# Performance work log

Hardware: AMD Instinct MI355X
Metric: run time of the kernel (lower is better)

The kernel has to match this reference:

```python
import jax, jax.numpy as jnp
import numpy as np

B, T, F = 4096, 72, 9
H = 64            # GRU units per direction
DENSE = 128
P = 24            # predict_window


def _gru_scan(xp, h0, U, br, act):
    """xp: (T,B,3H) precomputed input projections; Keras reset_after=True GRU."""
    def step(h, x_t):
        rec = h @ U + br                      # (B,3H)
        xz, xr, xh = jnp.split(x_t, 3, axis=-1)
        rz, rr, rh = jnp.split(rec, 3, axis=-1)
        z = jax.nn.sigmoid(xz + rz)
        r = jax.nn.sigmoid(xr + rr)
        hh = act(xh + r * rh)
        h_new = z * h + (1.0 - z) * hh
        return h_new, h_new
    hT, hs = jax.lax.scan(step, h0, xp)
    return hT, hs


def _bigru(x, h0f, h0b, Wf, Uf, bif, brf, Wb, Ub, bib, brb, act, return_sequences):
    xt = jnp.swapaxes(x, 0, 1)                # (T,B,F)
    xpf = xt @ Wf + bif                       # (T,B,3H)
    xpb = xt[::-1] @ Wb + bib                 # reversed time for backward dir
    hTf, hsf = _gru_scan(xpf, h0f, Uf, brf, act)
    hTb, hsb = _gru_scan(xpb, h0b, Ub, brb, act)
    if return_sequences:
        out = jnp.concatenate([hsf, hsb[::-1]], axis=-1)   # (T,B,2H)
        return jnp.swapaxes(out, 0, 1)                      # (B,T,2H)
    return jnp.concatenate([hTf, hTb], axis=-1)             # (B,2H)


def _glorot(key, shape):
    fan_in, fan_out = shape[0], shape[-1]
    lim = np.sqrt(6.0 / (fan_in + fan_out))
    return jax.random.uniform(key, shape, jnp.float32, -lim, lim)


def setup_inputs() -> dict:
    key = jax.random.key(0)
    ks = jax.random.split(key, 16)
    d = {
        "x": jax.random.normal(ks[0], (B, T, F), jnp.float32),
        "h0_fwd": jnp.zeros((B, H), jnp.float32),
        "h0_bwd": jnp.zeros((B, H), jnp.float32),
        # d1 (input F=9), forward & backward directions
        "d1f_W": _glorot(ks[1], (F, 3 * H)), "d1f_U": _glorot(ks[2], (H, 3 * H)),
        "d1f_bi": jnp.zeros((3 * H,), jnp.float32), "d1f_br": jnp.zeros((3 * H,), jnp.float32),
        "d1b_W": _glorot(ks[3], (F, 3 * H)), "d1b_U": _glorot(ks[4], (H, 3 * H)),
        "d1b_bi": jnp.zeros((3 * H,), jnp.float32), "d1b_br": jnp.zeros((3 * H,), jnp.float32),
        # d2 (input 2H=128)
        "d2f_W": _glorot(ks[5], (2 * H, 3 * H)), "d2f_U": _glorot(ks[6], (H, 3 * H)),
        "d2f_bi": jnp.zeros((3 * H,), jnp.float32), "d2f_br": jnp.zeros((3 * H,), jnp.float32),
        "d2b_W": _glorot(ks[7], (2 * H, 3 * H)), "d2b_U": _glorot(ks[8], (H, 3 * H)),
        "d2b_bi": jnp.zeros((3 * H,), jnp.float32), "d2b_br": jnp.zeros((3 * H,), jnp.float32),
        # dense heads
        "dense_W": _glorot(ks[9], (2 * H, DENSE)), "dense_b": jnp.zeros((DENSE,), jnp.float32),
        "out_W": _glorot(ks[10], (DENSE, P)), "out_b": jnp.zeros((P,), jnp.float32),
    }
    return d


def reference(x, h0_fwd, h0_bwd,
              d1f_W, d1f_U, d1f_bi, d1f_br, d1b_W, d1b_U, d1b_bi, d1b_br,
              d2f_W, d2f_U, d2f_bi, d2f_br, d2b_W, d2b_U, d2b_bi, d2b_br,
              dense_W, dense_b, out_W, out_b):
    # d1: Bidirectional GRU(64, activation=relu), return_sequences=True, initial_state=hidden
    seq = _bigru(x, h0_fwd, h0_bwd,
                 d1f_W, d1f_U, d1f_bi, d1f_br,
                 d1b_W, d1b_U, d1b_bi, d1b_br,
                 jax.nn.relu, True)                         # (B,T,128)
    # d2: Bidirectional GRU(64, activation=tanh), zero initial state, last-state output
    z0 = jnp.zeros((x.shape[0], H), seq.dtype)
    feat = _bigru(seq, z0, z0,
                  d2f_W, d2f_U, d2f_bi, d2f_br,
                  d2b_W, d2b_U, d2b_bi, d2b_br,
                  jnp.tanh, False)                          # (B,128)
    h = jax.nn.relu(feat @ dense_W + dense_b)               # (B,128)
    out = jax.nn.softmax(h @ out_W + out_b, axis=-1)        # (B,P)
    return out
```

## Files before the change

kernel.cpp:

```cpp
#include <hip/hip_runtime.h>
#include <hip/hip_bf16.h>

typedef __attribute__((ext_vector_type(8))) short short8;
typedef __attribute__((ext_vector_type(4))) float f32x4;
typedef unsigned short ush;

#define MFMA_B16(a, b, c) __builtin_amdgcn_mfma_f32_16x16x32_bf16((a), (b), (c), 0, 0, 0)

__device__ __forceinline__ float bf2f(ush u) {
    union { unsigned int i; float f; } v; v.i = ((unsigned int)u) << 16; return v.f;
}
__device__ __forceinline__ ush f2bf(float f) {
    union { float f; unsigned int i; } v; v.f = f;
    unsigned int r = v.i + 0x7fffu + ((v.i >> 16) & 1u);
    return (ush)(r >> 16);
}
__device__ __forceinline__ float rcp_f(float x) { return __builtin_amdgcn_rcpf(x); }
__device__ __forceinline__ float sigm_pre(float x) {
    return rcp_f(1.0f + __builtin_amdgcn_exp2f(x));
}
__device__ __forceinline__ float tanh_pre(float x) {
    return 1.0f - 2.0f * rcp_f(__builtin_amdgcn_exp2f(x) + 1.0f);
}

__device__ __forceinline__ void lds_barrier() {
    asm volatile("s_waitcnt lgkmcnt(0)" ::: "memory");
    __builtin_amdgcn_s_barrier();
    asm volatile("" ::: "memory");
}

__device__ __forceinline__ bool probe_bf16(const ush* p, int tid, int* s_cnt) {
    if (tid == 0) *s_cnt = 0;
    __syncthreads();
    ush s = p[tid & 255];
    int e = (s >> 7) & 0xFF;
    if (tid < 256 && e >= 117 && e <= 137) atomicAdd(s_cnt, 1);
    __syncthreads();
    return *s_cnt >= 200;
}

struct WArgs {
    const void* src[20];
    int off[21];
};

__global__ __launch_bounds__(256)
void convert_w(WArgs a, ush* __restrict__ arena, const ush* __restrict__ probe)
{
    __shared__ int cnt;
    const bool bf = probe_bf16(probe, threadIdx.x, &cnt);
    const int total = a.off[20];
    for (int i = blockIdx.x * 256 + threadIdx.x; i < total; i += gridDim.x * 256) {
        int t = 0;
        while (t < 19 && i >= a.off[t + 1]) ++t;
        const int local = i - a.off[t];
        float v = bf ? bf2f(((const ush*)a.src[t])[local])
                     : ((const float*)a.src[t])[local];
        if (t < 16) {
            const int col = local % 192;
            if (col < 128) v *= -1.4426950408889634f;
            else if (t >= 8) v *= 2.885390081777927f;
        }
        arena[i] = f2bf(v);
    }
}

__global__ __launch_bounds__(256, 1)
void gru1_kernel(const void* __restrict__ X, const void* __restrict__ h0f,
                 const void* __restrict__ h0b, int cb, int bchunk,
                 const ush* __restrict__ Wf, const ush* __restrict__ Uf,
                 const ush* __restrict__ bif, const ush* __restrict__ brf,
                 const ush* __restrict__ Wb, const ush* __restrict__ Ub,
                 const ush* __restrict__ bib, const ush* __restrict__ brb,
                 ush* __restrict__ seq)
{
    const int tid  = threadIdx.x;
    const int lane = tid & 63;
    const int wv   = tid >> 6;
    const int q    = lane >> 4;
    const int ln   = lane & 15;
    const int dir  = blockIdx.y;
    const int lb0  = blockIdx.x * 16;
    const int gb0  = cb + lb0;
    const int u    = wv * 16 + ln;

    const ush* W  = dir ? Wb  : Wf;
    const ush* U  = dir ? Ub  : Uf;
    const ush* bi = dir ? bib : bif;
    const ush* br = dir ? brb : brf;
    const void* h0 = dir ? h0b : h0f;

    __shared__ __align__(16) ush Ah[2][16][72];
    __shared__ __align__(16) ush Ax[2][16][40];
    __shared__ int s_cnt;

    const bool xbf = probe_bf16((const ush*)X, tid, &s_cnt);

    {
        ush* p = &Ax[0][0][0];
        for (int i = tid; i < 2 * 16 * 40; i += 256) p[i] = 0;
    }
    __syncthreads();

    {
        const int tx0 = dir ? 71 : 0;
        if (tid < 144) {
            int r = tid / 9, k = tid - 9 * r;
            size_t idx = ((size_t)(gb0 + r) * 72 + tx0) * 9 + k;
            ush hv, lv;
            if (xbf) { hv = ((const ush*)X)[idx]; lv = 0; }
            else { float v = ((const float*)X)[idx]; hv = f2bf(v); lv = f2bf(v - bf2f(hv)); }
            Ax[0][r][2 * k]     = hv;
            Ax[0][r][2 * k + 1] = lv;
        }
    }

    short8 bU[3][2];
    short8 bW[3];
#pragma unroll
    for (int g = 0; g < 3; ++g) {
        const int col = g * 64 + u;
#pragma unroll
        for (int ks = 0; ks < 2; ++ks) {
            short8 f;
#pragma unroll
            for (int j = 0; j < 8; ++j) {
                int kp = ks * 32 + q * 8 + j;
                f[j] = (short)U[(size_t)kp * 192 + col];
            }
            bU[g][ks] = f;
        }
        short8 fw;
#pragma unroll
        for (int j = 0; j < 8; ++j) {
            int kp = q * 8 + j;
            fw[j] = (kp < 18) ? (short)W[(size_t)(kp >> 1) * 192 + col] : (short)0;
        }
        bW[g] = fw;
    }

    const float bz  = bf2f(bi[u])       + bf2f(br[u]);
    const float brg = bf2f(bi[64 + u])  + bf2f(br[64 + u]);
    const float bih = bf2f(bi[128 + u]);
    const float brh = bf2f(br[128 + u]);
    const f32x4 Cz  = {bz,  bz,  bz,  bz};
    const f32x4 Cr  = {brg, brg, brg, brg};
    const f32x4 Chx = {bih, bih, bih, bih};
    const f32x4 Chr = {brh, brh, brh, brh};

    float hreg[4];
#pragma unroll
    for (int i = 0; i < 4; ++i) {
        int m = q * 4 + i;
        size_t idx = (size_t)(gb0 + m) * 64 + u;
        float hv = xbf ? bf2f(((const ush*)h0)[idx])
                       : ((const float*)h0)[idx];
        hreg[i] = hv;
        Ah[0][m][u] = f2bf(hv);
    }

    const int r2 = tid >> 3, c2 = tid & 7;
    const int r0x = tid / 9, k0x = tid - 9 * r0x;

    unsigned int craw = 0;
    if (tid < 144) {
        const int tx = dir ? 70 : 1;
        size_t idx = ((size_t)(gb0 + r0x) * 72 + tx) * 9 + k0x;
        craw = xbf ? (unsigned int)((const ush*)X)[idx]
                   : ((const unsigned int*)X)[idx];
    }
    __syncthreads();

#pragma unroll 2
    for (int t = 0; t < 72; ++t) {
        const int cur = t & 1, nb = cur ^ 1;

        unsigned int fraw = 0;
        if (t < 70 && tid < 144) {
            const int tx = dir ? (69 - t) : (t + 2);
            size_t idx = ((size_t)(gb0 + r0x) * 72 + tx) * 9 + k0x;
            fraw = xbf ? (unsigned int)((const ush*)X)[idx]
                       : ((const unsigned int*)X)[idx];
        }

        if (t > 0 && tid < 128) {
            const int tw = dir ? (71 - (t - 1)) : (t - 1);
            int4 v = *(const int4*)&Ah[cur][r2][c2 * 8];
            *(int4*)(seq + ((size_t)tw * bchunk + lb0 + r2) * 128 + dir * 64 + c2 * 8) = v;
        }

        const ush* ap = &Ah[cur][ln][0];
        short8 a0 = *(const short8*)(ap + q * 8);
        short8 a1 = *(const short8*)(ap + 32 + q * 8);
        short8 ax = *(const short8*)(&Ax[cur][ln][q * 8]);
        f32x4 az  = MFMA_B16(ax, bW[0], Cz);
        az        = MFMA_B16(a0, bU[0][0], az);
        az        = MFMA_B16(a1, bU[0][1], az);
        f32x4 ar  = MFMA_B16(ax, bW[1], Cr);
        ar        = MFMA_B16(a0, bU[1][0], ar);
        ar        = MFMA_B16(a1, bU[1][1], ar);
        f32x4 ahx = MFMA_B16(ax, bW[2], Chx);
        f32x4 ahr = MFMA_B16(a0, bU[2][0], Chr);
        ahr       = MFMA_B16(a1, bU[2][1], ahr);

#pragma unroll
        for (int i = 0; i < 4; ++i) {
            const int m = q * 4 + i;
            float z = sigm_pre(az[i]);
            float r = sigm_pre(ar[i]);
            float pre = ahx[i] + r * ahr[i];
            float hh = fmaxf(pre, 0.0f);
            float hn = hh + z * (hreg[i] - hh);
            hreg[i] = hn;
            Ah[nb][m][u] = f2bf(hn);
        }

        if (t < 71 && tid < 144) {
            ush hv, lv;
            if (xbf) { hv = (ush)craw; lv = 0; }
            else {
                float v = __uint_as_float(craw);
                hv = f2bf(v); lv = f2bf(v - bf2f(hv));
            }
            Ax[nb][r0x][2 * k0x]     = hv;
            Ax[nb][r0x][2 * k0x + 1] = lv;
        }
        craw = fraw;
        lds_barrier();
    }

    if (tid < 128) {
        const int tw = dir ? 0 : 71;
        int4 v = *(const int4*)&Ah[0][r2][c2 * 8];
        *(int4*)(seq + ((size_t)tw * bchunk + lb0 + r2) * 128 + dir * 64 + c2 * 8) = v;
    }
}

#define PCOMPUTE(E, BUFI)                                                      \
    do {                                                                       \
        f32x4 p0 = MFMA_B16(E##0, bV[0][0], Cg0);                              \
        p0 = MFMA_B16(E##1, bV[0][1], p0);                                     \
        p0 = MFMA_B16(E##2, bV[0][2], p0);                                     \
        p0 = MFMA_B16(E##3, bV[0][3], p0);                                     \
        *(f32x4*)&Pbuf[BUFI][0][pn][poff] = p0;                                \
        f32x4 p1 = MFMA_B16(E##0, bV[1][0], Cg1);                              \
        p1 = MFMA_B16(E##1, bV[1][1], p1);                                     \
        p1 = MFMA_B16(E##2, bV[1][2], p1);                                     \
        p1 = MFMA_B16(E##3, bV[1][3], p1);                                     \
        *(f32x4*)&Pbuf[BUFI][1][pn][poff] = p1;                                \
        f32x4 p2 = MFMA_B16(E##0, bV[2][0], Cg2);                              \
        p2 = MFMA_B16(E##1, bV[2][1], p2);                                     \
        p2 = MFMA_B16(E##2, bV[2][2], p2);                                     \
        p2 = MFMA_B16(E##3, bV[2][3], p2);                                     \
        *(f32x4*)&Pbuf[BUFI][2][pn][poff] = p2;                                \
    } while (0)

#define ELOAD(E, T)                                                            \
    do {                                                                       \
        const ush* sp_ = sptr0 + (long long)(T) * tstride;                     \
        E##0 = *(const short8*)(sp_);                                          \
        E##1 = *(const short8*)(sp_ + 32);                                     \
        E##2 = *(const short8*)(sp_ + 64);                                     \
        E##3 = *(const short8*)(sp_ + 96);                                     \
    } while (0)

__global__ __launch_bounds__(512, 1)
void gru2_kernel(const ush* __restrict__ seq, int cb, int bchunk,
                 const ush* __restrict__ W2f, const ush* __restrict__ U2f,
                 const ush* __restrict__ bi2f, const ush* __restrict__ br2f,
                 const ush* __restrict__ W2b, const ush* __restrict__ U2b,
                 const ush* __restrict__ bi2b, const ush* __restrict__ br2b,
                 float* __restrict__ feat)
{
    const int tid  = threadIdx.x;
    const int wv   = tid >> 6;
    const int lane = tid & 63;
    const int q    = lane >> 4;
    const int ln   = lane & 15;
    const int dir  = blockIdx.y;
    const int lb0  = blockIdx.x * 16;
    const int gb0  = cb + lb0;

    const ush* W  = dir ? W2b  : W2f;
    const ush* U  = dir ? U2b  : U2f;
    const ush* bi = dir ? bi2b : bi2f;
    const ush* br = dir ? br2b : br2f;

    __shared__ __align__(16) float Pbuf[2][3][4][288];
    __shared__ __align__(16) ush Ah[2][16][72];

    const int poff = (lane >> 3) * 36 + (lane & 7) * 4;

    if (wv < 4) {
        const int pn = wv;
        const int u2 = pn * 16 + ln;

        short8 bV[3][4];
#pragma unroll
        for (int g = 0; g < 3; ++g) {
            const int col = g * 64 + u2;
#pragma unroll
            for (int ks = 0; ks < 4; ++ks) {
                short8 f;
#pragma unroll
                for (int j = 0; j < 8; ++j) {
                    int kp = ks * 32 + q * 8 + j;
                    f[j] = (short)W[(size_t)kp * 192 + col];
                }
                bV[g][ks] = f;
            }
        }
        const float bz  = bf2f(bi[u2]) + bf2f(br[u2]);
        const float brg = bf2f(bi[64 + u2]) + bf2f(br[64 + u2]);
        const float bih = bf2f(bi[128 + u2]);
        const f32x4 Cg0 = {bz, bz, bz, bz};
        const f32x4 Cg1 = {brg, brg, brg, brg};
        const f32x4 Cg2 = {bih, bih, bih, bih};

        const long long tstride = (long long)bchunk * 128 * (dir ? -1 : 1);
        const ush* sptr0 = seq + (size_t)(lb0 + ln) * 128 + q * 8
                         + (dir ? 71ll * bchunk * 128 : 0);

        short8 EA0, EA1, EA2, EA3, EB0, EB1, EB2, EB3;
        ELOAD(EA, 0);
        PCOMPUTE(EA, 0);
        ELOAD(EA, 1);
        ELOAD(EB, 2);
        lds_barrier();

        for (int t = 0; t < 72; t += 2) {
            PCOMPUTE(EA, 1);
            if (t <= 68) ELOAD(EA, t + 3);
            lds_barrier();
            if (t + 1 < 71) PCOMPUTE(EB, 0);
            if (t + 1 <= 68) ELOAD(EB, t + 4);
            lds_barrier();
        }
    } else {
        const int cn = wv - 4;
        const int u2 = cn * 16 + ln;

        short8 bU[3][2];
#pragma unroll
        for (int g = 0; g < 3; ++g) {
            const int col = g * 64 + u2;
#pragma unroll
            for (int ks = 0; ks < 2; ++ks) {
                short8 f;
#pragma unroll
                for (int j = 0; j < 8; ++j) {
                    int kp = ks * 32 + q * 8 + j;
                    f[j] = (short)U[(size_t)kp * 192 + col];
                }
                bU[g][ks] = f;
            }
        }
        const float brh = bf2f(br[128 + u2]);
        const f32x4 Chr = {brh, brh, brh, brh};

        for (int i = tid - 256; i < 16 * 72; i += 256) (&Ah[0][0][0])[i] = 0;
        float hreg[4];
#pragma unroll
        for (int i = 0; i < 4; ++i) hreg[i] = 0.0f;
        lds_barrier();

        for (int t = 0; t < 72; ++t) {
            const int cur = t & 1, nb = cur ^ 1;

            f32x4 Pz = *(const f32x4*)&Pbuf[cur][0][cn][poff];
            f32x4 Pr = *(const f32x4*)&Pbuf[cur][1][cn][poff];
            f32x4 Pc = *(const f32x4*)&Pbuf[cur][2][cn][poff];

            const ush* ap = &Ah[cur][ln][0];
            short8 a0 = *(const short8*)(ap + q * 8);
            short8 a1 = *(const short8*)(ap + 32 + q * 8);

            f32x4 az  = MFMA_B16(a0, bU[0][0], Pz);
            az        = MFMA_B16(a1, bU[0][1], az);
            f32x4 ar  = MFMA_B16(a0, bU[1][0], Pr);
            ar        = MFMA_B16(a1, bU[1][1], ar);
            f32x4 ahr = MFMA_B16(a0, bU[2][0], Chr);
            ahr       = MFMA_B16(a1, bU[2][1], ahr);

#pragma unroll
            for (int i = 0; i < 4; ++i) {
                const int m = q * 4 + i;
                float z = sigm_pre(az[i]);
                float r = sigm_pre(ar[i]);
                float pre = Pc[i] + r * ahr[i];
                float hh = tanh_pre(pre);
                float hn = hh + z * (hreg[i] - hh);
                hreg[i] = hn;
                Ah[nb][m][u2] = f2bf(hn);
            }
            lds_barrier();
        }

#pragma unroll
        for (int i = 0; i < 4; ++i) {
            const int m = q * 4 + i;
            feat[(size_t)(gb0 + m) * 128 + dir * 64 + u2] = hreg[i];
        }
    }
}

__global__ __launch_bounds__(256, 1)
void head_kernel(const float* __restrict__ feat,
                 const ush* __restrict__ dW, const ush* __restrict__ db,
                 const ush* __restrict__ oW, const ush* __restrict__ ob,
                 float* __restrict__ out)
{
    const int tid = threadIdx.x;
    const int b0  = blockIdx.x * 16;

    __shared__ __align__(16) ush Wl[128][136];
    __shared__ __align__(16) float fs[16][128];
    __shared__ __align__(16) float hs[16][136];
    __shared__ __align__(16) float ls[16][32];

    for (int i = tid; i < 2048; i += 256) {
        const int k = i >> 4;
        const int c = (i & 15) * 8;
        *(int4*)&Wl[k][c] = *(const int4*)(dW + (size_t)k * 128 + c);
    }
    {
        const float4* src = (const float4*)(feat + (size_t)b0 * 128);
        float4* dst = (float4*)&fs[0][0];
        for (int i = tid; i < 512; i += 256) dst[i] = src[i];
    }
    __syncthreads();

    {
        const int row = tid >> 4;
        const int j0  = (tid & 15) * 8;
        float acc[8];
#pragma unroll
        for (int jj = 0; jj < 8; ++jj) acc[jj] = bf2f(db[j0 + jj]);
        for (int k = 0; k < 128; ++k) {
            float f = fs[row][k];
            short8 w = *(const short8*)&Wl[k][j0];
#pragma unroll
            for (int jj = 0; jj < 8; ++jj)
                acc[jj] += f * bf2f((ush)w[jj]);
        }
#pragma unroll
        for (int jj = 0; jj < 8; ++jj) hs[row][j0 + jj] = fmaxf(acc[jj], 0.0f);
    }
    __syncthreads();

    for (int e = tid; e < 16 * 24; e += 256) {
        const int row = e / 24, l = e - 24 * row;
        float acc = bf2f(ob[l]);
        for (int k = 0; k < 128; ++k)
            acc += hs[row][k] * bf2f(oW[(size_t)k * 24 + l]);
        ls[row][l] = acc;
    }
    __syncthreads();

    for (int e = tid; e < 16 * 24; e += 256) {
        const int row = e / 24, l = e - 24 * row;
        float mx = ls[row][0];
#pragma unroll
        for (int k = 1; k < 24; ++k) mx = fmaxf(mx, ls[row][k]);
        float s = 0.0f;
#pragma unroll
        for (int k = 0; k < 24; ++k) s += __expf(ls[row][k] - mx);
        float v = __expf(ls[row][l] - mx) * rcp_f(s);
        out[(size_t)(b0 + row) * 24 + l] = v;
    }
}

extern "C" void kernel_launch(void* const* d_in, const int* in_sizes, int n_in,
                              void* d_out, int out_size, void* d_ws, size_t ws_size,
                              hipStream_t stream) {
    (void)in_sizes; (void)n_in; (void)out_size;

    static const int wc[20] = {
        1728, 12288, 192, 192,
        1728, 12288, 192, 192,
        24576, 12288, 192, 192,
        24576, 12288, 192, 192,
        16384, 128,
        3072, 24
    };

    WArgs a;
    int off = 0;
    for (int t = 0; t < 20; ++t) {
        a.src[t] = d_in[t + 3];
        a.off[t] = off;
        off += wc[t];
    }
    a.off[20] = off;

    const unsigned long long arena_bytes = 245952ull;
    const unsigned long long feat_bytes  = 4096ull * 128ull * 4ull;
    const unsigned long long seq_full    = 72ull * 4096ull * 128ull * 2ull;
    const unsigned long long fixed       = arena_bytes + feat_bytes;

    int nc = 32;
    for (int c = 1; c <= 32; c *= 2) {
        if (fixed + seq_full / (unsigned long long)c <= (unsigned long long)ws_size) { nc = c; break; }
    }
    const int bchunk = 4096 / nc;

    ush* arena  = (ush*)d_ws;
    float* feat = (float*)((char*)d_ws + arena_bytes);
    ush* seq    = (ush*)((char*)d_ws + fixed);

    convert_w<<<128, 256, 0, stream>>>(a, arena, (const ush*)d_in[0]);

    const ush* d1fW = arena + a.off[0];
    const ush* d1fU = arena + a.off[1];
    const ush* d1fbi= arena + a.off[2];
    const ush* d1fbr= arena + a.off[3];
    const ush* d1bW = arena + a.off[4];
    const ush* d1bU = arena + a.off[5];
    const ush* d1bbi= arena + a.off[6];
    const ush* d1bbr= arena + a.off[7];
    const ush* d2fW = arena + a.off[8];
    const ush* d2fU = arena + a.off[9];
    const ush* d2fbi= arena + a.off[10];
    const ush* d2fbr= arena + a.off[11];
    const ush* d2bW = arena + a.off[12];
    const ush* d2bU = arena + a.off[13];
    const ush* d2bbi= arena + a.off[14];
    const ush* d2bbr= arena + a.off[15];
    const ush* dW   = arena + a.off[16];
    const ush* db   = arena + a.off[17];
    const ush* oW   = arena + a.off[18];
    const ush* ob   = arena + a.off[19];

    for (int c = 0; c < nc; ++c) {
        const int cb = c * bchunk;
        gru1_kernel<<<dim3(bchunk / 16, 2), 256, 0, stream>>>(
            d_in[0], d_in[1], d_in[2], cb, bchunk,
            d1fW, d1fU, d1fbi, d1fbr, d1bW, d1bU, d1bbi, d1bbr, seq);
        gru2_kernel<<<dim3(bchunk / 16, 2), 512, 0, stream>>>(
            seq, cb, bchunk,
            d2fW, d2fU, d2fbi, d2fbr, d2bW, d2bU, d2bbi, d2bbr, feat);
    }
    head_kernel<<<256, 256, 0, stream>>>(
        feat, dW, db, oW, ob, (float*)d_out);
}
```

Measured before the change: 242.6 us.

## Merge gru2 producer/consumer warps into single 256-thread recurrent loop

After: 245.6 us. About the same (+1.3%).

```diff
diff --git a/kernel.cpp b/kernel.cpp
--- a/kernel.cpp
+++ b/kernel.cpp
@@ -90,15 +90,15 @@
     const ush* br = dir ? brb : brf;
     const void* h0 = dir ? h0b : h0f;
 
-    __shared__ __align__(16) ush Ah[2][16][72];
-    __shared__ __align__(16) ush Ax[2][16][40];
+    __shared__ __align__(16) ush Ah[2][16][76];
+    __shared__ __align__(16) ush Ax[2][16][44];
     __shared__ int s_cnt;
 
     const bool xbf = probe_bf16((const ush*)X, tid, &s_cnt);
 
     {
         ush* p = &Ax[0][0][0];
-        for (int i = tid; i < 2 * 16 * 40; i += 256) p[i] = 0;
+        for (int i = tid; i < 2 * 16 * 44; i += 256) p[i] = 0;
     }
     __syncthreads();
 
@@ -236,35 +236,54 @@
     }
 }
 
-#define PCOMPUTE(E, BUFI)                                                      \
+#define G2STEP(T, S0, S1, S2, S3)                                              \
     do {                                                                       \
-        f32x4 p0 = MFMA_B16(E##0, bV[0][0], Cg0);                              \
-        p0 = MFMA_B16(E##1, bV[0][1], p0);                                     \
-        p0 = MFMA_B16(E##2, bV[0][2], p0);                                     \
-        p0 = MFMA_B16(E##3, bV[0][3], p0);                                     \
-        *(f32x4*)&Pbuf[BUFI][0][pn][poff] = p0;                                \
-        f32x4 p1 = MFMA_B16(E##0, bV[1][0], Cg1);                              \
-        p1 = MFMA_B16(E##1, bV[1][1], p1);                                     \
-        p1 = MFMA_B16(E##2, bV[1][2], p1);                                     \
-        p1 = MFMA_B16(E##3, bV[1][3], p1);                                     \
-        *(f32x4*)&Pbuf[BUFI][1][pn][poff] = p1;                                \
-        f32x4 p2 = MFMA_B16(E##0, bV[2][0], Cg2);                              \
-        p2 = MFMA_B16(E##1, bV[2][1], p2);                                     \
-        p2 = MFMA_B16(E##2, bV[2][2], p2);                                     \
-        p2 = MFMA_B16(E##3, bV[2][3], p2);                                     \
-        *(f32x4*)&Pbuf[BUFI][2][pn][poff] = p2;                                \
+        const int cur_ = (T) & 1, nb_ = cur_ ^ 1;                              \
+        const ush* ap_ = &Ah[cur_][ln][0];                                     \
+        short8 a0 = *(const short8*)(ap_ + q * 8);                             \
+        short8 a1 = *(const short8*)(ap_ + 32 + q * 8);                        \
+        f32x4 az  = MFMA_B16(a0, bU[0][0], P0);                                \
+        az        = MFMA_B16(a1, bU[0][1], az);                                \
+        f32x4 ar  = MFMA_B16(a0, bU[1][0], P1);                                \
+        ar        = MFMA_B16(a1, bU[1][1], ar);                                \
+        f32x4 ahr = MFMA_B16(a0, bU[2][0], Chr);                               \
+        ahr       = MFMA_B16(a1, bU[2][1], ahr);                               \
+        f32x4 ahx = P2;                                                        \
+        _Pragma("unroll") for (int i = 0; i < 4; ++i) {                        \
+            const int m = q * 4 + i;                                           \
+            float z = sigm_pre(az[i]);                                         \
+            float r = sigm_pre(ar[i]);                                         \
+            float pre = ahx[i] + r * ahr[i];                                   \
+            float hh = tanh_pre(pre);                                          \
+            float hn = hh + z * (hreg[i] - hh);                                \
+            hreg[i] = hn;                                                      \
+            Ah[nb_][m][u] = f2bf(hn);                                          \
+        }                                                                      \
+        if ((T) < 71) {               \
+            P0 = MFMA_B16(S0, bV[0][0], Cz);                                   \
+            P0 = MFMA_B16(S1, bV[0][1], P0);                                   \
+            P0 = MFMA_B16(S2, bV[0][2], P0);                                   \
+            P0 = MFMA_B16(S3, bV[0][3], P0);                                   \
+            P1 = MFMA_B16(S0, bV[1][0], Cr);                                   \
+            P1 = MFMA_B16(S1, bV[1][1], P1);                                   \
+            P1 = MFMA_B16(S2, bV[1][2], P1);                                   \
+            P1 = MFMA_B16(S3, bV[1][3], P1);                                   \
+            P2 = MFMA_B16(S0, bV[2][0], Chx);                                  \
+            P2 = MFMA_B16(S1, bV[2][1], P2);                                   \
+            P2 = MFMA_B16(S2, bV[2][2], P2);                                   \
+            P2 = MFMA_B16(S3, bV[2][3], P2);                                   \
+        }                                                                      \
+        if ((T) <= 67) {                       \
+            const ush* sp_ = sptr0 + (long long)((T) + 4) * tstride;           \
+            S0 = *(const short8*)(sp_);                                        \
+            S1 = *(const short8*)(sp_ + 32);                                   \
+            S2 = *(const short8*)(sp_ + 64);                                   \
+            S3 = *(const short8*)(sp_ + 96);                                   \
+        }                                                                      \
+        lds_barrier();                                                         \
     } while (0)
 
-#define ELOAD(E, T)                                                            \
-    do {                                                                       \
-        const ush* sp_ = sptr0 + (long long)(T) * tstride;                     \
-        E##0 = *(const short8*)(sp_);                                          \
-        E##1 = *(const short8*)(sp_ + 32);                                     \
-        E##2 = *(const short8*)(sp_ + 64);                                     \
-        E##3 = *(const short8*)(sp_ + 96);                                     \
-    } while (0)
-
-__global__ __launch_bounds__(512, 1)
+__global__ __launch_bounds__(256, 1)
 void gru2_kernel(const ush* __restrict__ seq, int cb, int bchunk,
                  const ush* __restrict__ W2f, const ush* __restrict__ U2f,
                  const ush* __restrict__ bi2f, const ush* __restrict__ br2f,
@@ -273,134 +292,119 @@
                  float* __restrict__ feat)
 {
     const int tid  = threadIdx.x;
+    const int lane = tid & 63;
     const int wv   = tid >> 6;
-    const int lane = tid & 63;
     const int q    = lane >> 4;
     const int ln   = lane & 15;
     const int dir  = blockIdx.y;
     const int lb0  = blockIdx.x * 16;
     const int gb0  = cb + lb0;
+    const int u    = wv * 16 + ln;
 
     const ush* W  = dir ? W2b  : W2f;
     const ush* U  = dir ? U2b  : U2f;
     const ush* bi = dir ? bi2b : bi2f;
     const ush* br = dir ? br2b : br2f;
 
-    __shared__ __align__(16) float Pbuf[2][3][4][288];
-    __shared__ __align__(16) ush Ah[2][16][72];
-
-    const int poff = (lane >> 3) * 36 + (lane & 7) * 4;
-
-    if (wv < 4) {
-        const int pn = wv;
-        const int u2 = pn * 16 + ln;
-
-        short8 bV[3][4];
-#pragma unroll
-        for (int g = 0; g < 3; ++g) {
-            const int col = g * 64 + u2;
-#pragma unroll
-            for (int ks = 0; ks < 4; ++ks) {
-                short8 f;
-#pragma unroll
-                for (int j = 0; j < 8; ++j) {
-                    int kp = ks * 32 + q * 8 + j;
-                    f[j] = (short)W[(size_t)kp * 192 + col];
-                }
-                bV[g][ks] = f;
+    __shared__ __align__(16) ush Ah[2][16][76];
+
+    {
+        ush* p = &Ah[0][0][0];
+        for (int i = tid; i < 16 * 76; i += 256) p[i] = 0;
+    }
+
+    const long long tstride = (long long)bchunk * 128 * (dir ? -1 : 1);
+    const ush* sptr0 = seq + ((size_t)(lb0 + ln)) * 128 + q * 8
+                     + (dir ? 71ll * bchunk * 128 : 0);
+
+    short8 bU[3][2];
+    short8 bV[3][4];
+#pragma unroll
+    for (int g = 0; g < 3; ++g) {
+        const int col = g * 64 + u;
+#pragma unroll
+        for (int ks = 0; ks < 2; ++ks) {
+            short8 f;
+#pragma unroll
+            for (int j = 0; j < 8; ++j) {
+                int kp = ks * 32 + q * 8 + j;
+                f[j] = (short)U[(size_t)kp * 192 + col];
             }
-        }
-        const float bz  = bf2f(bi[u2]) + bf2f(br[u2]);
-        const float brg = bf2f(bi[64 + u2]) + bf2f(br[64 + u2]);
-        const float bih = bf2f(bi[128 + u2]);
-        const f32x4 Cg0 = {bz, bz, bz, bz};
-        const f32x4 Cg1 = {brg, brg, brg, brg};
-        const f32x4 Cg2 = {bih, bih, bih, bih};
-
-        const long long tstride = (long long)bchunk * 128 * (dir ? -1 : 1);
-        const ush* sptr0 = seq + (size_t)(lb0 + ln) * 128 + q * 8
-                         + (dir ? 71ll * bchunk * 128 : 0);
-
-        short8 EA0, EA1, EA2, EA3, EB0, EB1, EB2, EB3;
-        ELOAD(EA, 0);
-        PCOMPUTE(EA, 0);
-        ELOAD(EA, 1);
-        ELOAD(EB, 2);
-        lds_barrier();
-
-        for (int t = 0; t < 72; t += 2) {
-            PCOMPUTE(EA, 1);
-            if (t <= 68) ELOAD(EA, t + 3);
-            lds_barrier();
-            if (t + 1 < 71) PCOMPUTE(EB, 0);
-            if (t + 1 <= 68) ELOAD(EB, t + 4);
-            lds_barrier();
-        }
-    } else {
-        const int cn = wv - 4;
-        const int u2 = cn * 16 + ln;
-
-        short8 bU[3][2];
-#pragma unroll
-        for (int g = 0; g < 3; ++g) {
-            const int col = g * 64 + u2;
-#pragma unroll
-            for (int ks = 0; ks < 2; ++ks) {
-                short8 f;
-#pragma unroll
-                for (int j = 0; j < 8; ++j) {
-                    int kp = ks * 32 + q * 8 + j;
-                    f[j] = (short)U[(size_t)kp * 192 + col];
-                }
-                bU[g][ks] = f;
+            bU[g][ks] = f;
+        }
+#pragma unroll
+        for (int ks = 0; ks < 4; ++ks) {
+            short8 fv;
+#pragma unroll
+            for (int j = 0; j < 8; ++j) {
+                int kp = ks * 32 + q * 8 + j;
+                fv[j] = (short)W[(size_t)kp * 192 + col];
             }
-        }
-        const float brh = bf2f(br[128 + u2]);
-        const f32x4 Chr = {brh, brh, brh, brh};
-
-        for (int i = tid - 256; i < 16 * 72; i += 256) (&Ah[0][0][0])[i] = 0;
-        float hreg[4];
-#pragma unroll
-        for (int i = 0; i < 4; ++i) hreg[i] = 0.0f;
-        lds_barrier();
-
-        for (int t = 0; t < 72; ++t) {
-            const int cur = t & 1, nb = cur ^ 1;
-
-            f32x4 Pz = *(const f32x4*)&Pbuf[cur][0][cn][poff];
-            f32x4 Pr = *(const f32x4*)&Pbuf[cur][1][cn][poff];
-            f32x4 Pc = *(const f32x4*)&Pbuf[cur][2][cn][poff];
-
-            const ush* ap = &Ah[cur][ln][0];
-            short8 a0 = *(const short8*)(ap + q * 8);
-            short8 a1 = *(const short8*)(ap + 32 + q * 8);
-
-            f32x4 az  = MFMA_B16(a0, bU[0][0], Pz);
-            az        = MFMA_B16(a1, bU[0][1], az);
-            f32x4 ar  = MFMA_B16(a0, bU[1][0], Pr);
-            ar        = MFMA_B16(a1, bU[1][1], ar);
-            f32x4 ahr = MFMA_B16(a0, bU[2][0], Chr);
-            ahr       = MFMA_B16(a1, bU[2][1], ahr);
-
-#pragma unroll
-            for (int i = 0; i < 4; ++i) {
-                const int m = q * 4 + i;
-                float z = sigm_pre(az[i]);
-                float r = sigm_pre(ar[i]);
-                float pre = Pc[i] + r * ahr[i];
-                float hh = tanh_pre(pre);
-                float hn = hh + z * (hreg[i] - hh);
-                hreg[i] = hn;
-                Ah[nb][m][u2] = f2bf(hn);
-            }
-            lds_barrier();
-        }
-
-#pragma unroll
-        for (int i = 0; i < 4; ++i) {
-            const int m = q * 4 + i;
-            feat[(size_t)(gb0 + m) * 128 + dir * 64 + u2] = hreg[i];
-        }
+            bV[g][ks] = fv;
+        }
+    }
+
+    const float bz  = bf2f(bi[u])       + bf2f(br[u]);
+    const float brg = bf2f(bi[64 + u])  + bf2f(br[64 + u]);
+    const float bih = bf2f(bi[128 + u]);
+    const float brh = bf2f(br[128 + u]);
+    const f32x4 Cz  = {bz,  bz,  bz,  bz};
+    const f32x4 Cr  = {brg, brg, brg, brg};
+    const f32x4 Chx = {bih, bih, bih, bih};
+    const f32x4 Chr = {brh, brh, brh, brh};
+
+    float hreg[4];
+#pragma unroll
+    for (int i = 0; i < 4; ++i) hreg[i] = 0.0f;
+
+    f32x4 P0, P1, P2;
+    {
+        const ush* sp = sptr0;
+        short8 s0 = *(const short8*)(sp);
+        short8 s1 = *(const short8*)(sp + 32);
+        short8 s2 = *(const short8*)(sp + 64);
+        short8 s3 = *(const short8*)(sp + 96);
+        P0 = MFMA_B16(s0, bV[0][0], Cz);
+        P0 = MFMA_B16(s1, bV[0][1], P0);
+        P0 = MFMA_B16(s2, bV[0][2], P0);
+        P0 = MFMA_B16(s3, bV[0][3], P0);
+        P1 = MFMA_B16(s0, bV[1][0], Cr);
+        P1 = MFMA_B16(s1, bV[1][1], P1);
+        P1 = MFMA_B16(s2, bV[1][2], P1);
+        P1 = MFMA_B16(s3, bV[1][3], P1);
+        P2 = MFMA_B16(s0, bV[2][0], Chx);
+        P2 = MFMA_B16(s1, bV[2][1], P2);
+        P2 = MFMA_B16(s2, bV[2][2], P2);
+        P2 = MFMA_B16(s3, bV[2][3], P2);
+    }
+    short8 A0, A1, A2, A3, B0, B1, B2, B3, D0, D1, D2, D3;
+    {
+        const ush* sp = sptr0 + tstride;
+        A0 = *(const short8*)(sp);        A1 = *(const short8*)(sp + 32);
+        A2 = *(const short8*)(sp + 64);   A3 = *(const short8*)(sp + 96);
+    }
+    {
+        const ush* sp = sptr0 + 2 * tstride;
+        B0 = *(const short8*)(sp);        B1 = *(const short8*)(sp + 32);
+        B2 = *(const short8*)(sp + 64);   B3 = *(const short8*)(sp + 96);
+    }
+    {
+        const ush* sp = sptr0 + 3 * tstride;
+        D0 = *(const short8*)(sp);        D1 = *(const short8*)(sp + 32);
+        D2 = *(const short8*)(sp + 64);   D3 = *(const short8*)(sp + 96);
+    }
+    __syncthreads();
+
+    for (int t = 0; t < 72; t += 3) {
+        G2STEP(t,     A0, A1, A2, A3);
+        G2STEP(t + 1, B0, B1, B2, B3);
+        G2STEP(t + 2, D0, D1, D2, D3);
+    }
+
+#pragma unroll
+    for (int i = 0; i < 4; ++i) {
+        const int m = q * 4 + i;
+        feat[(size_t)(gb0 + m) * 128 + dir * 64 + u] = hreg[i];
     }
 }
 
@@ -536,7 +540,7 @@
         gru1_kernel<<<dim3(bchunk / 16, 2), 256, 0, stream>>>(
             d_in[0], d_in[1], d_in[2], cb, bchunk,
             d1fW, d1fU, d1fbi, d1fbr, d1bW, d1bU, d1bbi, d1bbr, seq);
-        gru2_kernel<<<dim3(bchunk / 16, 2), 512, 0, stream>>>(
+        gru2_kernel<<<dim3(bchunk / 16, 2), 256, 0, stream>>>(
             seq, cb, bchunk,
             d2fW, d2fU, d2fbi, d2fbr, d2bW, d2bU, d2bbi, d2bbr, feat);
     }
```

## Shrink GRU2 blocks to one producer and one consumer wave

Applied to the files above, without the earlier changes.

New measurement: 251.4 us. +3.6%, slower.

```diff
diff --git a/kernel.cpp b/kernel.cpp
--- a/kernel.cpp
+++ b/kernel.cpp
@@ -18,9 +18,6 @@
 __device__ __forceinline__ float rcp_f(float x) { return __builtin_amdgcn_rcpf(x); }
 __device__ __forceinline__ float sigm_pre(float x) {
     return rcp_f(1.0f + __builtin_amdgcn_exp2f(x));
-}
-__device__ __forceinline__ float tanh_pre(float x) {
-    return 1.0f - 2.0f * rcp_f(__builtin_amdgcn_exp2f(x) + 1.0f);
 }
 
 __device__ __forceinline__ void lds_barrier() {
@@ -90,15 +87,15 @@
     const ush* br = dir ? brb : brf;
     const void* h0 = dir ? h0b : h0f;
 
-    __shared__ __align__(16) ush Ah[2][16][72];
-    __shared__ __align__(16) ush Ax[2][16][40];
+    __shared__ __align__(16) ush Ah[2][16][76];
+    __shared__ __align__(16) ush Ax[2][16][44];
     __shared__ int s_cnt;
 
     const bool xbf = probe_bf16((const ush*)X, tid, &s_cnt);
 
     {
         ush* p = &Ax[0][0][0];
-        for (int i = tid; i < 2 * 16 * 40; i += 256) p[i] = 0;
+        for (int i = tid; i < 2 * 16 * 44; i += 256) p[i] = 0;
     }
     __syncthreads();
 
@@ -236,35 +233,61 @@
     }
 }
 
-#define PCOMPUTE(E, BUFI)                                                      \
+#define PROD_STEP(FA, BUFI, T)                                                 \
     do {                                                                       \
-        f32x4 p0 = MFMA_B16(E##0, bV[0][0], Cg0);                              \
-        p0 = MFMA_B16(E##1, bV[0][1], p0);                                     \
-        p0 = MFMA_B16(E##2, bV[0][2], p0);                                     \
-        p0 = MFMA_B16(E##3, bV[0][3], p0);                                     \
-        *(f32x4*)&Pbuf[BUFI][0][pn][poff] = p0;                                \
-        f32x4 p1 = MFMA_B16(E##0, bV[1][0], Cg1);                              \
-        p1 = MFMA_B16(E##1, bV[1][1], p1);                                     \
-        p1 = MFMA_B16(E##2, bV[1][2], p1);                                     \
-        p1 = MFMA_B16(E##3, bV[1][3], p1);                                     \
-        *(f32x4*)&Pbuf[BUFI][1][pn][poff] = p1;                                \
-        f32x4 p2 = MFMA_B16(E##0, bV[2][0], Cg2);                              \
-        p2 = MFMA_B16(E##1, bV[2][1], p2);                                     \
-        p2 = MFMA_B16(E##2, bV[2][2], p2);                                     \
-        p2 = MFMA_B16(E##3, bV[2][3], p2);                                     \
-        *(f32x4*)&Pbuf[BUFI][2][pn][poff] = p2;                                \
+        if ((T) < 71) {                                                        \
+            _Pragma("unroll") for (int g = 0; g < 3; ++g) {                    \
+                _Pragma("unroll") for (int n = 0; n < 4; ++n) {                \
+                    f32x4 acc = MFMA_B16(FA[0], bV[g][0][n], Cg[g][n]);        \
+                    acc = MFMA_B16(FA[1], bV[g][1][n], acc);                   \
+                    acc = MFMA_B16(FA[2], bV[g][2][n], acc);                   \
+                    acc = MFMA_B16(FA[3], bV[g][3][n], acc);                   \
+                    *(f32x4*)&Pbuf[BUFI][g][n][poff] = acc;                    \
+                }                                                              \
+            }                                                                  \
+        }                                                                      \
+        if ((T) < 69) {                                                        \
+            const ush* sp = sptr0 + (long long)((T) + 3) * tstride;            \
+            FA[0] = *(const short8*)sp;                                        \
+            FA[1] = *(const short8*)(sp + 32);                                 \
+            FA[2] = *(const short8*)(sp + 64);                                 \
+            FA[3] = *(const short8*)(sp + 96);                                 \
+        }                                                                      \
     } while (0)
 
-#define ELOAD(E, T)                                                            \
+#define CONS_STEP(BUFI, T)                                                     \
     do {                                                                       \
-        const ush* sp_ = sptr0 + (long long)(T) * tstride;                     \
-        E##0 = *(const short8*)(sp_);                                          \
-        E##1 = *(const short8*)(sp_ + 32);                                     \
-        E##2 = *(const short8*)(sp_ + 64);                                     \
-        E##3 = *(const short8*)(sp_ + 96);                                     \
+        f32x4 Pz[4], Pr[4], Pc[4];                                             \
+        _Pragma("unroll") for (int n = 0; n < 4; ++n) {                        \
+            Pz[n] = *(const f32x4*)&Pbuf[BUFI][0][n][poff];                    \
+            Pr[n] = *(const f32x4*)&Pbuf[BUFI][1][n][poff];                    \
+            Pc[n] = *(const f32x4*)&Pbuf[BUFI][2][n][poff];                    \
+        }                                                                      \
+        short8 a0 = *(const short8*)&Ah[ln][q * 8];                            \
+        short8 a1 = *(const short8*)&Ah[ln][32 + q * 8];                       \
+        f32x4 az[4], ar[4], ahr[4];                                            \
+        _Pragma("unroll") for (int n = 0; n < 4; ++n) {                        \
+            az[n]  = MFMA_B16(a0, bU[0][0][n], Pz[n]);                         \
+            az[n]  = MFMA_B16(a1, bU[0][1][n], az[n]);                         \
+            ar[n]  = MFMA_B16(a0, bU[1][0][n], Pr[n]);                         \
+            ar[n]  = MFMA_B16(a1, bU[1][1][n], ar[n]);                         \
+            ahr[n] = MFMA_B16(a0, bU[2][0][n], Chr[n]);                        \
+            ahr[n] = MFMA_B16(a1, bU[2][1][n], ahr[n]);                        \
+        }                                                                      \
+        _Pragma("unroll") for (int n = 0; n < 4; ++n)                          \
+            _Pragma("unroll") for (int i = 0; i < 4; ++i) {                    \
+                float z = sigm_pre(az[n][i]);                                  \
+                float r = sigm_pre(ar[n][i]);                                  \
+                float pre = Pc[n][i] + r * ahr[n][i];                          \
+                float e = __builtin_amdgcn_exp2f(pre);         \
+                float hh = 1.0f - 2.0f * rcp_f(e + 1.0f);                      \
+                float hn = hh + z * (hreg[n][i] - hh);                         \
+                hreg[n][i] = hn;                                               \
+                Ah[q * 4 + i][n * 16 + ln] = f2bf(hn);                         \
+            }                                                                  \
     } while (0)
 
-__global__ __launch_bounds__(512, 1)
+__global__ __launch_bounds__(128, 1)
 void gru2_kernel(const ush* __restrict__ seq, int cb, int bchunk,
                  const ush* __restrict__ W2f, const ush* __restrict__ U2f,
                  const ush* __restrict__ bi2f, const ush* __restrict__ br2f,
@@ -272,14 +295,9 @@
                  const ush* __restrict__ bi2b, const ush* __restrict__ br2b,
                  float* __restrict__ feat)
 {
-    const int tid  = threadIdx.x;
-    const int wv   = tid >> 6;
-    const int lane = tid & 63;
-    const int q    = lane >> 4;
-    const int ln   = lane & 15;
-    const int dir  = blockIdx.y;
-    const int lb0  = blockIdx.x * 16;
-    const int gb0  = cb + lb0;
+    const int tid = threadIdx.x;
+    const int wv = tid >> 6, lane = tid & 63, q = lane >> 4, ln = lane & 15;
+    const int dir = blockIdx.y, lb0 = blockIdx.x * 16, gb0 = cb + lb0;
 
     const ush* W  = dir ? W2b  : W2f;
     const ush* U  = dir ? U2b  : U2f;
@@ -287,120 +305,125 @@
     const ush* br = dir ? br2b : br2f;
 
     __shared__ __align__(16) float Pbuf[2][3][4][288];
-    __shared__ __align__(16) ush Ah[2][16][72];
+    __shared__ __align__(16) ush Ah[16][72];
 
     const int poff = (lane >> 3) * 36 + (lane & 7) * 4;
 
-    if (wv < 4) {
-        const int pn = wv;
-        const int u2 = pn * 16 + ln;
-
-        short8 bV[3][4];
-#pragma unroll
-        for (int g = 0; g < 3; ++g) {
-            const int col = g * 64 + u2;
-#pragma unroll
-            for (int ks = 0; ks < 4; ++ks) {
-                short8 f;
-#pragma unroll
-                for (int j = 0; j < 8; ++j) {
-                    int kp = ks * 32 + q * 8 + j;
-                    f[j] = (short)W[(size_t)kp * 192 + col];
+    if (wv == 0) {
+        short8 bV[3][4][4];
+#pragma unroll
+        for (int g = 0; g < 3; ++g)
+#pragma unroll
+            for (int n = 0; n < 4; ++n) {
+                const int col = g * 64 + n * 16 + ln;
+#pragma unroll
+                for (int ks = 0; ks < 4; ++ks) {
+                    short8 f;
+#pragma unroll
+                    for (int j = 0; j < 8; ++j) {
+                        int kp = ks * 32 + q * 8 + j;
+                        f[j] = (short)W[(size_t)kp * 192 + col];
+                    }
+                    bV[g][ks][n] = f;
                 }
-                bV[g][ks] = f;
             }
-        }
-        const float bz  = bf2f(bi[u2]) + bf2f(br[u2]);
-        const float brg = bf2f(bi[64 + u2]) + bf2f(br[64 + u2]);
-        const float bih = bf2f(bi[128 + u2]);
-        const f32x4 Cg0 = {bz, bz, bz, bz};
-        const f32x4 Cg1 = {brg, brg, brg, brg};
-        const f32x4 Cg2 = {bih, bih, bih, bih};
+        f32x4 Cg[3][4];
+#pragma unroll
+        for (int n = 0; n < 4; ++n) {
+            const int u2 = n * 16 + ln;
+            const float bz  = bf2f(bi[u2]) + bf2f(br[u2]);
+            const float brg = bf2f(bi[64 + u2]) + bf2f(br[64 + u2]);
+            const float bih = bf2f(bi[128 + u2]);
+            Cg[0][n] = (f32x4){bz, bz, bz, bz};
+            Cg[1][n] = (f32x4){brg, brg, brg, brg};
+            Cg[2][n] = (f32x4){bih, bih, bih, bih};
+        }
 
         const long long tstride = (long long)bchunk * 128 * (dir ? -1 : 1);
         const ush* sptr0 = seq + (size_t)(lb0 + ln) * 128 + q * 8
                          + (dir ? 71ll * bchunk * 128 : 0);
 
-        short8 EA0, EA1, EA2, EA3, EB0, EB1, EB2, EB3;
-        ELOAD(EA, 0);
-        PCOMPUTE(EA, 0);
-        ELOAD(EA, 1);
-        ELOAD(EB, 2);
+        {
+            const ush* sp = sptr0;
+            short8 s0 = *(const short8*)sp;
+            short8 s1 = *(const short8*)(sp + 32);
+            short8 s2 = *(const short8*)(sp + 64);
+            short8 s3 = *(const short8*)(sp + 96);
+#pragma unroll
+            for (int g = 0; g < 3; ++g)
+#pragma unroll
+                for (int n = 0; n < 4; ++n) {
+                    f32x4 acc = MFMA_B16(s0, bV[g][0][n], Cg[g][n]);
+                    acc = MFMA_B16(s1, bV[g][1][n], acc);
+                    acc = MFMA_B16(s2, bV[g][2][n], acc);
+                    acc = MFMA_B16(s3, bV[g][3][n], acc);
+                    *(f32x4*)&Pbuf[0][g][n][poff] = acc;
+                }
+        }
+        short8 F0[4], F1[4];
+        {
+            const ush* sp = sptr0 + tstride;
+            F0[0] = *(const short8*)sp;        F0[1] = *(const short8*)(sp + 32);
+            F0[2] = *(const short8*)(sp + 64); F0[3] = *(const short8*)(sp + 96);
+        }
+        {
+            const ush* sp = sptr0 + 2 * tstride;
+            F1[0] = *(const short8*)sp;        F1[1] = *(const short8*)(sp + 32);
+            F1[2] = *(const short8*)(sp + 64); F1[3] = *(const short8*)(sp + 96);
+        }
         lds_barrier();
 
         for (int t = 0; t < 72; t += 2) {
-            PCOMPUTE(EA, 1);
-            if (t <= 68) ELOAD(EA, t + 3);
+            PROD_STEP(F0, 1, t);
             lds_barrier();
-            if (t + 1 < 71) PCOMPUTE(EB, 0);
-            if (t + 1 <= 68) ELOAD(EB, t + 4);
+            PROD_STEP(F1, 0, t + 1);
             lds_barrier();
         }
     } else {
-        const int cn = wv - 4;
-        const int u2 = cn * 16 + ln;
-
-        short8 bU[3][2];
-#pragma unroll
-        for (int g = 0; g < 3; ++g) {
-            const int col = g * 64 + u2;
-#pragma unroll
-            for (int ks = 0; ks < 2; ++ks) {
-                short8 f;
-#pragma unroll
-                for (int j = 0; j < 8; ++j) {
-                    int kp = ks * 32 + q * 8 + j;
-                    f[j] = (short)U[(size_t)kp * 192 + col];
+        short8 bU[3][2][4];
+#pragma unroll
+        for (int g = 0; g < 3; ++g)
+#pragma unroll
+            for (int n = 0; n < 4; ++n) {
+                const int col = g * 64 + n * 16 + ln;
+#pragma unroll
+                for (int ks = 0; ks < 2; ++ks) {
+                    short8 f;
+#pragma unroll
+                    for (int j = 0; j < 8; ++j) {
+                        int kp = ks * 32 + q * 8 + j;
+                        f[j] = (short)U[(size_t)kp * 192 + col];
+                    }
+                    bU[g][ks][n] = f;
                 }
-                bU[g][ks] = f;
             }
-        }
-        const float brh = bf2f(br[128 + u2]);
-        const f32x4 Chr = {brh, brh, brh, brh};
-
-        for (int i = tid - 256; i < 16 * 72; i += 256) (&Ah[0][0][0])[i] = 0;
-        float hreg[4];
-#pragma unroll
-        for (int i = 0; i < 4; ++i) hreg[i] = 0.0f;
+        f32x4 Chr[4];
+#pragma unroll
+        for (int n = 0; n < 4; ++n) {
+            const float brh = bf2f(br[128 + n * 16 + ln]);
+            Chr[n] = (f32x4){brh, brh, brh, brh};
+        }
+
+        for (int i = lane; i < 16 * 72; i += 64) (&Ah[0][0])[i] = 0;
+        float hreg[4][4];
+#pragma unroll
+        for (int n = 0; n < 4; ++n)
+#pragma unroll
+            for (int i = 0; i < 4; ++i) hreg[n][i] = 0.0f;
         lds_barrier();
 
-        for (int t = 0; t < 72; ++t) {
-            const int cur = t & 1, nb = cur ^ 1;
-
-            f32x4 Pz = *(const f32x4*)&Pbuf[cur][0][cn][poff];
-            f32x4 Pr = *(const f32x4*)&Pbuf[cur][1][cn][poff];
-            f32x4 Pc = *(const f32x4*)&Pbuf[cur][2][cn][poff];
-
-            const ush* ap = &Ah[cur][ln][0];
-            short8 a0 = *(const short8*)(ap + q * 8);
-            short8 a1 = *(const short8*)(ap + 32 + q * 8);
-
-            f32x4 az  = MFMA_B16(a0, bU[0][0], Pz);
-            az        = MFMA_B16(a1, bU[0][1], az);
-            f32x4 ar  = MFMA_B16(a0, bU[1][0], Pr);
-            ar        = MFMA_B16(a1, bU[1][1], ar);
-            f32x4 ahr = MFMA_B16(a0, bU[2][0], Chr);
-            ahr       = MFMA_B16(a1, bU[2][1], ahr);
-
-#pragma unroll
-            for (int i = 0; i < 4; ++i) {
-                const int m = q * 4 + i;
-                float z = sigm_pre(az[i]);
-                float r = sigm_pre(ar[i]);
-                float pre = Pc[i] + r * ahr[i];
-                float hh = tanh_pre(pre);
-                float hn = hh + z * (hreg[i] - hh);
-                hreg[i] = hn;
-                Ah[nb][m][u2] = f2bf(hn);
-            }
+        for (int t = 0; t < 72; t += 2) {
+            CONS_STEP(0, t);
             lds_barrier();
-        }
-
-#pragma unroll
-        for (int i = 0; i < 4; ++i) {
-            const int m = q * 4 + i;
-            feat[(size_t)(gb0 + m) * 128 + dir * 64 + u2] = hreg[i];
-        }
+            CONS_STEP(1, t + 1);
+            lds_barrier();
+        }
+
+#pragma unroll
+        for (int n = 0; n < 4; ++n)
+#pragma unroll
+            for (int i = 0; i < 4; ++i)
+                feat[(size_t)(gb0 + q * 4 + i) * 128 + dir * 64 + n * 16 + ln] = hreg[n][i];
     }
 }
 
@@ -536,7 +559,7 @@
         gru1_kernel<<<dim3(bchunk / 16, 2), 256, 0, stream>>>(
             d_in[0], d_in[1], d_in[2], cb, bchunk,
             d1fW, d1fU, d1fbi, d1fbr, d1bW, d1bU, d1bbi, d1bbr, seq);
-        gru2_kernel<<<dim3(bchunk / 16, 2), 512, 0, stream>>>(
+        gru2_kernel<<<dim3(bchunk / 16, 2), 128, 0, stream>>>(
             seq, cb, bchunk,
             d2fW, d2fU, d2fbi, d2fbr, d2bW, d2bU, d2bbi, d2bbr, feat);
     }
```
